# Kernel tuning notes

Measured on AMD Instinct MI355X. Metric: run time of the kernel, lower is better.

The kernel has to match this reference:

```python
import jax, jax.numpy as jnp
import numpy as np
import math

N_HEADS = 16

def _rope_tables(T, D, dtype):
    # inv_freq over even dims, emb = [freqs, freqs] -> [T, D]
    inv_freq = 1.0 / (10000.0 ** (jnp.arange(0, D, 2, dtype=jnp.float32) / D))
    freqs = jnp.arange(T, dtype=jnp.float32)[:, None] * inv_freq[None, :]  # [T, D/2]
    emb = jnp.concatenate([freqs, freqs], axis=-1)  # [T, D]
    return jnp.cos(emb).astype(dtype), jnp.sin(emb).astype(dtype)

def _rotate_half(x):
    d = x.shape[-1] // 2
    return jnp.concatenate([-x[..., d:], x[..., :d]], axis=-1)

def setup_inputs() -> dict:
    key = jax.random.key(0)
    ks = jax.random.split(key, 5)
    B, T, C = 2, 2048, 1024
    s = 1.0 / math.sqrt(C)
    return {
        "x": jax.random.normal(ks[0], (B, T, C), dtype=jnp.float32),
        "Wq": jax.random.normal(ks[1], (C, C), dtype=jnp.float32) * s,
        "Wk": jax.random.normal(ks[2], (C, C), dtype=jnp.float32) * s,
        "Wv": jax.random.normal(ks[3], (C, C), dtype=jnp.float32) * s,
        "Wo": jax.random.normal(ks[4], (C, C), dtype=jnp.float32) * s,
    }

def reference(x, Wq, Wk, Wv, Wo):
    B, T, C = x.shape
    H = N_HEADS
    D = C // H
    # QKV projections (torch Linear, bias=False: y = x @ W.T), split into heads
    def proj(W):
        return (x @ W.T).reshape(B, T, H, D).transpose(0, 2, 1, 3)  # [B,H,T,D]
    q, k, v = proj(Wq), proj(Wk), proj(Wv)
    # RoPE
    cos, sin = _rope_tables(T, D, x.dtype)  # [T,D] each, broadcast over B,H
    q = q * cos + _rotate_half(q) * sin
    k = k * cos + _rotate_half(k) * sin
    # scaled dot-product attention with causal mask
    scale = 1.0 / math.sqrt(D)
    attn = jnp.einsum('bhtd,bhsd->bhts', q, k) * scale  # [B,H,T,T]
    row = jnp.arange(T)[:, None]
    col = jnp.arange(T)[None, :]
    attn = jnp.where(col > row, -jnp.inf, attn)
    p = jax.nn.softmax(attn, axis=-1)
    out = jnp.einsum('bhts,bhsd->bhtd', p, v)  # [B,H,T,D]
    out = out.transpose(0, 2, 1, 3).reshape(B, T, C)
    return out @ Wo.T
```

## Files before the change

### kernel.cpp

```cpp
#include <hip/hip_runtime.h>
#include <hip/hip_bf16.h>


typedef __hip_bfloat16 bf16;
typedef __attribute__((ext_vector_type(8))) short bf16x8;
typedef __attribute__((ext_vector_type(4))) float f32x4;
typedef __attribute__((ext_vector_type(4))) short short4v;

#define MFMA16(a, b, c) __builtin_amdgcn_mfma_f32_16x16x32_bf16((a), (b), (c), 0, 0, 0)

constexpr int Bn = 2, Hn = 16, Tn = 2048, Dn = 64, Cn = 1024;
constexpr size_t NE = (size_t)Bn * Tn * Cn;
constexpr size_t WE = (size_t)Cn * Cn;
constexpr float QSCALE = 0.125f * 1.44269504088896f;
constexpr int PS = 68;

__device__ inline unsigned short bfbits(float x) {
    bf16 b = __float2bfloat16(x);
    return *(unsigned short*)&b;
}

__device__ inline bf16x8 pack8(f32x4 a, f32x4 b) {
    bf16x8 r;
#pragma unroll
    for (int i = 0; i < 4; ++i) r[i] = (short)bfbits(a[i]);
#pragma unroll
    for (int i = 0; i < 4; ++i) r[4 + i] = (short)bfbits(b[i]);
    return r;
}

__global__ __launch_bounds__(256) void convert_kernel(
    const float* __restrict__ x, const float* __restrict__ wq,
    const float* __restrict__ wk, const float* __restrict__ wv,
    const float* __restrict__ wo, bf16* __restrict__ dst)
{
    int blk = blockIdx.x;
    int lane = threadIdx.x & 63;
    int lx = lane & 15, quad = lane >> 4;
    const float* src;
    size_t doff;
    if (blk < 2048) {
        int frag = blk * 4 + (threadIdx.x >> 6);
        int mt = frag >> 5, kc = frag & 31;
        src = x + (size_t)(mt * 16 + lx) * Cn + kc * 32 + quad * 8;
        doff = (size_t)frag * 512 + lane * 8;
    } else {
        int w = (blk - 2048) >> 9, b = (blk - 2048) & 511;
        const float* s4[4] = {wq, wk, wv, wo};
        int frag = b * 4 + (threadIdx.x >> 6);
        int nb = frag >> 5, kc = frag & 31;
        src = s4[w] + (size_t)(nb * 16 + lx) * Cn + kc * 32 + quad * 8;
        doff = NE + (size_t)w * WE + (size_t)frag * 512 + lane * 8;
    }
    f32x4 a = *(const f32x4*)(src);
    f32x4 b2 = *(const f32x4*)(src + 4);
    *(bf16x8*)(dst + doff) = pack8(a, b2);
}

__global__ __launch_bounds__(256) void gemm_qkv_kernel(
    const bf16* __restrict__ Xf, const bf16* __restrict__ Wbase,
    bf16* __restrict__ Qo, bf16* __restrict__ Ko, bf16* __restrict__ Vo)
{
    const int bm = blockIdx.x, bn = blockIdx.y, wsel = blockIdx.z;
    const bf16* W = Wbase + (size_t)wsel * WE;
    const int tid  = threadIdx.x;
    const int wave = tid >> 6, lane = tid & 63;
    const int lx   = lane & 15, quad = lane >> 4;
    const int wm = wave >> 1, wn = wave & 1;

    const int mt0 = bm * 8 + wm * 4;
    const int nb0 = bn * 8 + wn * 4;
    const bf16* afrag = Xf + (size_t)mt0 * 32 * 512 + (size_t)lane * 8;
    const bf16* wfrag = W + (size_t)nb0 * 32 * 512 + (size_t)lane * 8;

    f32x4 acc[4][4] = {};
    bf16x8 acur[4], bcur[4], anxt[4], bnxt[4];
#pragma unroll
    for (int i = 0; i < 4; ++i) {
        acur[i] = *(const bf16x8*)(afrag + (size_t)i * 32 * 512);
        bcur[i] = *(const bf16x8*)(wfrag + (size_t)i * 32 * 512);
    }
    for (int kc = 0; kc < 32; ++kc) {
        if (kc < 31) {
#pragma unroll
            for (int i = 0; i < 4; ++i) {
                anxt[i] = *(const bf16x8*)(afrag + ((size_t)i * 32 + kc + 1) * 512);
                bnxt[i] = *(const bf16x8*)(wfrag + ((size_t)i * 32 + kc + 1) * 512);
            }
        }
#pragma unroll
        for (int mt = 0; mt < 4; ++mt)
#pragma unroll
            for (int nt = 0; nt < 4; ++nt)
                acc[mt][nt] = MFMA16(acur[mt], bcur[nt], acc[mt][nt]);
#pragma unroll
        for (int i = 0; i < 4; ++i) { acur[i] = anxt[i]; bcur[i] = bnxt[i]; }
    }

    const int h = bn * 2 + wn;
    if (wsel <= 1) {
#pragma unroll
        for (int mt = 0; mt < 4; ++mt)
#pragma unroll
            for (int r = 0; r < 4; ++r) {
                int mg = bm * 128 + wm * 64 + mt * 16 + quad * 4 + r;
                int t  = mg & (Tn - 1);
#pragma unroll
                for (int nt = 0; nt < 2; ++nt) {
                    int d = nt * 16 + lx;
                    float ang = (float)t * __expf(-(float)d * 0.2878231366f);
                    float c, s;
                    __sincosf(ang, &s, &c);
                    float a0 = acc[mt][nt][r], a1 = acc[mt][nt + 2][r];
                    acc[mt][nt][r]     = a0 * c - a1 * s;
                    acc[mt][nt + 2][r] = a1 * c + a0 * s;
                }
            }
    }

#pragma unroll
    for (int mt = 0; mt < 4; ++mt) {
        int mg0 = bm * 128 + wm * 64 + mt * 16 + quad * 4;
        int b = mg0 >> 11, tlo = mg0 & (Tn - 1);
        if (wsel == 0) {
#pragma unroll
            for (int nt = 0; nt < 4; ++nt)
#pragma unroll
                for (int r = 0; r < 4; ++r) {
                    int d = nt * 16 + lx;
                    Qo[((size_t)(b * Hn + h) * Tn + tlo + r) * Dn + d] =
                        __float2bfloat16(acc[mt][nt][r] * QSCALE);
                }
        } else if (wsel == 1) {
            bf16* Kf = Ko + (size_t)(b * Hn + h) * Tn * Dn;
            int c = tlo >> 6, ntk = (tlo >> 4) & 3;
#pragma unroll
            for (int nt = 0; nt < 4; ++nt) {
                size_t base = ((size_t)(c * 4 + ntk) * 2 + (nt >> 1)) * 512
                            + (size_t)((nt & 1) * 2 + (lx >> 3)) * 128
                            + (size_t)(tlo & 15) * 8 + (lx & 7);
#pragma unroll
                for (int r = 0; r < 4; ++r)
                    Kf[base + (size_t)r * 8] = __float2bfloat16(acc[mt][nt][r]);
            }
        } else {
            bf16* Vf = Vo + (size_t)(b * Hn + h) * Tn * Dn;
            int c = tlo >> 6, ksv = (tlo >> 5) & 1;
            int qv = (tlo >> 3) & 3, pos0 = tlo & 7;
#pragma unroll
            for (int nt = 0; nt < 4; ++nt) {
                short4v pk;
#pragma unroll
                for (int r = 0; r < 4; ++r) pk[r] = (short)bfbits(acc[mt][nt][r]);
                *(short4v*)&Vf[((size_t)(c * 8 + nt * 2 + ksv)) * 512
                               + (size_t)qv * 128 + (size_t)lx * 8 + pos0] = pk;
            }
        }
    }
}

__global__ __launch_bounds__(256) void gemm_out_kernel(
    const bf16* __restrict__ Af, const bf16* __restrict__ W, float* __restrict__ Out)
{
    const int bm = blockIdx.x, bn = blockIdx.y;
    const int tid  = threadIdx.x;
    const int wave = tid >> 6, lane = tid & 63;
    const int lx   = lane & 15, quad = lane >> 4;
    const int wm = wave >> 1, wn = wave & 1;

    const int mt0 = bm * 8 + wm * 4;
    const int nb0 = bn * 8 + wn * 4;
    const bf16* afrag = Af + (size_t)mt0 * 32 * 512 + (size_t)lane * 8;
    const bf16* wfrag = W + (size_t)nb0 * 32 * 512 + (size_t)lane * 8;

    f32x4 acc[4][4] = {};
    bf16x8 acur[4], bcur[4], anxt[4], bnxt[4];
#pragma unroll
    for (int i = 0; i < 4; ++i) {
        acur[i] = *(const bf16x8*)(afrag + (size_t)i * 32 * 512);
        bcur[i] = *(const bf16x8*)(wfrag + (size_t)i * 32 * 512);
    }
    for (int kc = 0; kc < 32; ++kc) {
        if (kc < 31) {
#pragma unroll
            for (int i = 0; i < 4; ++i) {
                anxt[i] = *(const bf16x8*)(afrag + ((size_t)i * 32 + kc + 1) * 512);
                bnxt[i] = *(const bf16x8*)(wfrag + ((size_t)i * 32 + kc + 1) * 512);
            }
        }
#pragma unroll
        for (int mt = 0; mt < 4; ++mt)
#pragma unroll
            for (int nt = 0; nt < 4; ++nt)
                acc[mt][nt] = MFMA16(acur[mt], bcur[nt], acc[mt][nt]);
#pragma unroll
        for (int i = 0; i < 4; ++i) { acur[i] = anxt[i]; bcur[i] = bnxt[i]; }
    }
#pragma unroll
    for (int mt = 0; mt < 4; ++mt)
#pragma unroll
        for (int nt = 0; nt < 4; ++nt)
#pragma unroll
            for (int r = 0; r < 4; ++r) {
                int mg = bm * 128 + wm * 64 + mt * 16 + quad * 4 + r;
                int ng = bn * 128 + wn * 64 + nt * 16 + lx;
                Out[(size_t)mg * Cn + ng] = acc[mt][nt][r];
            }
}

__global__ __launch_bounds__(256, 2) void attn_kernel(
    const bf16* __restrict__ Q, const bf16* __restrict__ K,
    const bf16* __restrict__ Vt, bf16* __restrict__ O)
{
    __shared__ unsigned short Pl[4][16 * PS];
    const int g  = blockIdx.x;
    const int bh = g & 31;
    const int p  = g >> 5;
    const int tHi = 31 - p, tLo = p;
    const int tid  = threadIdx.x;
    const int wave = tid >> 6, lane = tid & 63;
    const int lx   = lane & 15, quad = lane >> 4;

    const bf16* Qh = Q  + (size_t)bh * Tn * Dn;
    const bf16* Kh = K  + (size_t)bh * Tn * Dn;
    const bf16* Vh = Vt + (size_t)bh * Tn * Dn;
    unsigned short* pw = &Pl[wave][0];

    const int qrowH = tHi * 64 + wave * 16 + lx;
    bf16x8 aqH0 = *(const bf16x8*)(Qh + (size_t)qrowH * Dn + quad * 8);
    bf16x8 aqH1 = *(const bf16x8*)(Qh + (size_t)qrowH * Dn + 32 + quad * 8);
    const int qrowL = tLo * 64 + wave * 16 + lx;
    bf16x8 aqL0 = *(const bf16x8*)(Qh + (size_t)qrowL * Dn + quad * 8);
    bf16x8 aqL1 = *(const bf16x8*)(Qh + (size_t)qrowL * Dn + 32 + quad * 8);

    bf16x8 ones;
#pragma unroll
    for (int i = 0; i < 8; ++i) ones[i] = (short)0x3F80;

    f32x4 acc_oH[4] = {}, acc_oL[4] = {};
    f32x4 acc_lH = {},    acc_lL = {};
    const int row_local = wave * 16 + quad * 4;

    auto storeP = [&](const f32x4* accs, bool diag) {
        if (!diag) {
#pragma unroll
            for (int nt = 0; nt < 4; ++nt)
#pragma unroll
                for (int r = 0; r < 4; ++r)
                    pw[(quad * 4 + r) * PS + nt * 16 + lx] = bfbits(exp2f(accs[nt][r]));
        } else {
#pragma unroll
            for (int nt = 0; nt < 4; ++nt) {
                int keyl = nt * 16 + lx;
#pragma unroll
                for (int r = 0; r < 4; ++r) {
                    float pv = (keyl > row_local + r) ? 0.0f : exp2f(accs[nt][r]);
                    pw[(quad * 4 + r) * PS + nt * 16 + lx] = bfbits(pv);
                }
            }
        }
    };

    for (int c = 0; c <= tHi; ++c) {
        const bf16* kp = Kh + (size_t)c * 4096 + lane * 8;
        const bf16* vp = Vh + (size_t)c * 4096 + lane * 8;
        bf16x8 k[8], v[8];
#pragma unroll
        for (int i = 0; i < 8; ++i) {
            k[i] = *(const bf16x8*)(kp + (size_t)i * 512);
            v[i] = *(const bf16x8*)(vp + (size_t)i * 512);
        }
        const bool lo = (c <= tLo);
        f32x4 accsH[4] = {};
#pragma unroll
        for (int nt = 0; nt < 4; ++nt) {
            accsH[nt] = MFMA16(aqH0, k[nt * 2], accsH[nt]);
            accsH[nt] = MFMA16(aqH1, k[nt * 2 + 1], accsH[nt]);
        }
        f32x4 accsL[4] = {};
        if (lo) {
#pragma unroll
            for (int nt = 0; nt < 4; ++nt) {
                accsL[nt] = MFMA16(aqL0, k[nt * 2], accsL[nt]);
                accsL[nt] = MFMA16(aqL1, k[nt * 2 + 1], accsL[nt]);
            }
        }
        storeP(accsH, c == tHi);
        asm volatile("s_waitcnt lgkmcnt(0)" ::: "memory");
        {
            bf16x8 ap0 = *(const bf16x8*)&pw[lx * PS + quad * 8];
            bf16x8 ap1 = *(const bf16x8*)&pw[lx * PS + 32 + quad * 8];
            acc_lH = MFMA16(ap0, ones, acc_lH);
            acc_lH = MFMA16(ap1, ones, acc_lH);
#pragma unroll
            for (int dt = 0; dt < 4; ++dt) {
                acc_oH[dt] = MFMA16(ap0, v[dt * 2], acc_oH[dt]);
                acc_oH[dt] = MFMA16(ap1, v[dt * 2 + 1], acc_oH[dt]);
            }
        }
        if (lo) {
            storeP(accsL, c == tLo);
            asm volatile("s_waitcnt lgkmcnt(0)" ::: "memory");
            bf16x8 ap0 = *(const bf16x8*)&pw[lx * PS + quad * 8];
            bf16x8 ap1 = *(const bf16x8*)&pw[lx * PS + 32 + quad * 8];
            acc_lL = MFMA16(ap0, ones, acc_lL);
            acc_lL = MFMA16(ap1, ones, acc_lL);
#pragma unroll
            for (int dt = 0; dt < 4; ++dt) {
                acc_oL[dt] = MFMA16(ap0, v[dt * 2], acc_oL[dt]);
                acc_oL[dt] = MFMA16(ap1, v[dt * 2 + 1], acc_oL[dt]);
            }
        }
    }

    const int b = bh >> 4, h = bh & 15;
    auto writeO = [&](int t, const f32x4* acc_o, const f32x4& acc_l) {
        const int mtile = b * 128 + t * 4 + wave;
#pragma unroll
        for (int dt = 0; dt < 4; ++dt) {
            int ch = h * 64 + dt * 16 + lx;
            size_t base = ((size_t)mtile * 32 + (ch >> 5)) * 512
                        + (size_t)(((ch >> 3) & 3) * 16) * 8 + (ch & 7);
#pragma unroll
            for (int r = 0; r < 4; ++r) {
                float o = acc_o[dt][r] / acc_l[r];
                O[base + (size_t)(quad * 4 + r) * 8] = __float2bfloat16(o);
            }
        }
    };
    writeO(tHi, acc_oH, acc_lH);
    writeO(tLo, acc_oL, acc_lL);
}

extern "C" void kernel_launch(void* const* d_in, const int* in_sizes, int n_in,
                              void* d_out, int out_size, void* d_ws, size_t ws_size,
                              hipStream_t stream)
{
    const float* x  = (const float*)d_in[0];
    const float* Wq = (const float*)d_in[1];
    const float* Wk = (const float*)d_in[2];
    const float* Wv = (const float*)d_in[3];
    const float* Wo = (const float*)d_in[4];
    float* out = (float*)d_out;

    bf16* ws = (bf16*)d_ws;
    bf16* Xf = ws;
    bf16* Wb = ws + NE;
    bf16* Qb = ws + NE + 4 * WE;
    bf16* Kb = Qb + NE;
    bf16* Vb = Kb + NE;
    bf16* Ab = Xf;

    convert_kernel<<<4096, 256, 0, stream>>>(x, Wq, Wk, Wv, Wo, ws);
    gemm_qkv_kernel<<<dim3(32, 8, 3), 256, 0, stream>>>(Xf, Wb, Qb, Kb, Vb);
    attn_kernel<<<512, 256, 0, stream>>>(Qb, Kb, Vb, Ab);
    gemm_out_kernel<<<dim3(32, 8), 256, 0, stream>>>(Ab, Wb + 3 * WE, out);
}
```

Before: 178.0 us.

## Split attention KV loop across two wave groups with LDS reduction

```diff
diff --git a/kernel.cpp b/kernel.cpp
--- a/kernel.cpp
+++ b/kernel.cpp
@@ -14,6 +14,7 @@
 constexpr size_t WE = (size_t)Cn * Cn;
 constexpr float QSCALE = 0.125f * 1.44269504088896f;
 constexpr int PS = 68;
+constexpr int CS = 66;
 
 __device__ inline unsigned short bfbits(float x) {
     bf16 b = __float2bfloat16(x);
@@ -208,28 +209,31 @@
             }
 }
 
-__global__ __launch_bounds__(256, 2) void attn_kernel(
+__global__ __launch_bounds__(512, 4) void attn_kernel(
     const bf16* __restrict__ Q, const bf16* __restrict__ K,
     const bf16* __restrict__ Vt, bf16* __restrict__ O)
 {
-    __shared__ unsigned short Pl[4][16 * PS];
+    __shared__ unsigned short Pl[8][16 * PS];
+    __shared__ float Cb[4][16 * CS];
     const int g  = blockIdx.x;
     const int bh = g & 31;
     const int p  = g >> 5;
     const int tHi = 31 - p, tLo = p;
     const int tid  = threadIdx.x;
     const int wave = tid >> 6, lane = tid & 63;
+    const int w4   = wave & 3, half = wave >> 2;
     const int lx   = lane & 15, quad = lane >> 4;
 
     const bf16* Qh = Q  + (size_t)bh * Tn * Dn;
     const bf16* Kh = K  + (size_t)bh * Tn * Dn;
     const bf16* Vh = Vt + (size_t)bh * Tn * Dn;
     unsigned short* pw = &Pl[wave][0];
-
-    const int qrowH = tHi * 64 + wave * 16 + lx;
+    float* cb = &Cb[w4][0];
+
+    const int qrowH = tHi * 64 + w4 * 16 + lx;
     bf16x8 aqH0 = *(const bf16x8*)(Qh + (size_t)qrowH * Dn + quad * 8);
     bf16x8 aqH1 = *(const bf16x8*)(Qh + (size_t)qrowH * Dn + 32 + quad * 8);
-    const int qrowL = tLo * 64 + wave * 16 + lx;
+    const int qrowL = tLo * 64 + w4 * 16 + lx;
     bf16x8 aqL0 = *(const bf16x8*)(Qh + (size_t)qrowL * Dn + quad * 8);
     bf16x8 aqL1 = *(const bf16x8*)(Qh + (size_t)qrowL * Dn + 32 + quad * 8);
 
@@ -239,7 +243,7 @@
 
     f32x4 acc_oH[4] = {}, acc_oL[4] = {};
     f32x4 acc_lH = {},    acc_lL = {};
-    const int row_local = wave * 16 + quad * 4;
+    const int row_local = w4 * 16 + quad * 4;
 
     auto storeP = [&](const f32x4* accs, bool diag) {
         if (!diag) {
@@ -261,7 +265,7 @@
         }
     };
 
-    for (int c = 0; c <= tHi; ++c) {
+    for (int c = half; c <= tHi; c += 2) {
         const bf16* kp = Kh + (size_t)c * 4096 + lane * 8;
         const bf16* vp = Vh + (size_t)c * 4096 + lane * 8;
         bf16x8 k[8], v[8];
@@ -286,7 +290,6 @@
             }
         }
         storeP(accsH, c == tHi);
-        asm volatile("s_waitcnt lgkmcnt(0)" ::: "memory");
         {
             bf16x8 ap0 = *(const bf16x8*)&pw[lx * PS + quad * 8];
             bf16x8 ap1 = *(const bf16x8*)&pw[lx * PS + 32 + quad * 8];
@@ -300,7 +303,6 @@
         }
         if (lo) {
             storeP(accsL, c == tLo);
-            asm volatile("s_waitcnt lgkmcnt(0)" ::: "memory");
             bf16x8 ap0 = *(const bf16x8*)&pw[lx * PS + quad * 8];
             bf16x8 ap1 = *(const bf16x8*)&pw[lx * PS + 32 + quad * 8];
             acc_lL = MFMA16(ap0, ones, acc_lL);
@@ -315,7 +317,7 @@
 
     const int b = bh >> 4, h = bh & 15;
     auto writeO = [&](int t, const f32x4* acc_o, const f32x4& acc_l) {
-        const int mtile = b * 128 + t * 4 + wave;
+        const int mtile = b * 128 + t * 4 + w4;
 #pragma unroll
         for (int dt = 0; dt < 4; ++dt) {
             int ch = h * 64 + dt * 16 + lx;
@@ -328,8 +330,35 @@
             }
         }
     };
-    writeO(tHi, acc_oH, acc_lH);
-    writeO(tLo, acc_oL, acc_lL);
+    auto putC = [&](const f32x4* acc_o, const f32x4& acc_l) {
+#pragma unroll
+        for (int dt = 0; dt < 4; ++dt)
+#pragma unroll
+            for (int r = 0; r < 4; ++r)
+                cb[(quad * 4 + r) * CS + dt * 16 + lx] = acc_o[dt][r];
+        if (lx == 0)
+#pragma unroll
+            for (int r = 0; r < 4; ++r)
+                cb[(quad * 4 + r) * CS + 64] = acc_l[r];
+    };
+    auto addC = [&](f32x4* acc_o, f32x4& acc_l) {
+#pragma unroll
+        for (int dt = 0; dt < 4; ++dt)
+#pragma unroll
+            for (int r = 0; r < 4; ++r)
+                acc_o[dt][r] += cb[(quad * 4 + r) * CS + dt * 16 + lx];
+#pragma unroll
+        for (int r = 0; r < 4; ++r)
+            acc_l[r] += cb[(quad * 4 + r) * CS + 64];
+    };
+
+    if (half == 1) putC(acc_oH, acc_lH);
+    __syncthreads();
+    if (half == 0) { addC(acc_oH, acc_lH); writeO(tHi, acc_oH, acc_lH); }
+    __syncthreads();
+    if (half == 1) putC(acc_oL, acc_lL);
+    __syncthreads();
+    if (half == 0) { addC(acc_oL, acc_lL); writeO(tLo, acc_oL, acc_lL); }
 }
 
 extern "C" void kernel_launch(void* const* d_in, const int* in_sizes, int n_in,
@@ -353,6 +382,6 @@
 
     convert_kernel<<<4096, 256, 0, stream>>>(x, Wq, Wk, Wv, Wo, ws);
     gemm_qkv_kernel<<<dim3(32, 8, 3), 256, 0, stream>>>(Xf, Wb, Qb, Kb, Vb);
-    attn_kernel<<<512, 256, 0, stream>>>(Qb, Kb, Vb, Ab);
+    attn_kernel<<<512, 512, 0, stream>>>(Qb, Kb, Vb, Ab);
     gemm_out_kernel<<<dim3(32, 8), 256, 0, stream>>>(Ab, Wb + 3 * WE, out);
 }
```

New measurement: 241.5 us. +35.7%, slower.

## Split attention KV loop across two blocks and combine partials in a separate kernel

Applied to the files above, without the earlier changes.

```diff
diff --git a/kernel.cpp b/kernel.cpp
--- a/kernel.cpp
+++ b/kernel.cpp
@@ -208,14 +208,16 @@
             }
 }
 
-__global__ __launch_bounds__(256, 2) void attn_kernel(
+__global__ __launch_bounds__(256, 4) void attn_kernel(
     const bf16* __restrict__ Q, const bf16* __restrict__ K,
-    const bf16* __restrict__ Vt, bf16* __restrict__ O)
+    const bf16* __restrict__ Vt, float* __restrict__ Opart,
+    float* __restrict__ lpart)
 {
     __shared__ unsigned short Pl[4][16 * PS];
     const int g  = blockIdx.x;
     const int bh = g & 31;
-    const int p  = g >> 5;
+    const int p  = (g >> 5) & 15;
+    const int s  = g >> 9;
     const int tHi = 31 - p, tLo = p;
     const int tid  = threadIdx.x;
     const int wave = tid >> 6, lane = tid & 63;
@@ -261,7 +263,7 @@
         }
     };
 
-    for (int c = 0; c <= tHi; ++c) {
+    for (int c = s; c <= tHi; c += 2) {
         const bf16* kp = Kh + (size_t)c * 4096 + lane * 8;
         const bf16* vp = Vh + (size_t)c * 4096 + lane * 8;
         bf16x8 k[8], v[8];
@@ -313,23 +315,49 @@
         }
     }
 
+    const int pairIdx = g & 511;
+    float* Op = Opart + ((size_t)pairIdx * 2 + s) * 8192;
+    float* lp = lpart + ((size_t)pairIdx * 2 + s) * 128;
+    auto storePart = [&](int roff, const f32x4* acc_o, const f32x4& acc_l) {
+#pragma unroll
+        for (int dt = 0; dt < 4; ++dt)
+#pragma unroll
+            for (int r = 0; r < 4; ++r)
+                Op[(size_t)(roff + wave * 16 + quad * 4 + r) * 64 + dt * 16 + lx]
+                    = acc_o[dt][r];
+        if (lx == 0)
+#pragma unroll
+            for (int r = 0; r < 4; ++r)
+                lp[roff + wave * 16 + quad * 4 + r] = acc_l[r];
+    };
+    storePart(0, acc_oH, acc_lH);
+    storePart(64, acc_oL, acc_lL);
+}
+
+__global__ __launch_bounds__(256) void attn_combine_kernel(
+    const float* __restrict__ Opart, const float* __restrict__ lpart,
+    bf16* __restrict__ O)
+{
+    const int pair = blockIdx.x;
+    const int bh = pair & 31, p = pair >> 5;
+    const int tHi = 31 - p, tLo = p;
     const int b = bh >> 4, h = bh & 15;
-    auto writeO = [&](int t, const f32x4* acc_o, const f32x4& acc_l) {
-        const int mtile = b * 128 + t * 4 + wave;
-#pragma unroll
-        for (int dt = 0; dt < 4; ++dt) {
-            int ch = h * 64 + dt * 16 + lx;
-            size_t base = ((size_t)mtile * 32 + (ch >> 5)) * 512
-                        + (size_t)(((ch >> 3) & 3) * 16) * 8 + (ch & 7);
-#pragma unroll
-            for (int r = 0; r < 4; ++r) {
-                float o = acc_o[dt][r] / acc_l[r];
-                O[base + (size_t)(quad * 4 + r) * 8] = __float2bfloat16(o);
-            }
-        }
-    };
-    writeO(tHi, acc_oH, acc_lH);
-    writeO(tLo, acc_oL, acc_lL);
+    const float* O0 = Opart + (size_t)pair * 2 * 8192;
+    const float* O1 = O0 + 8192;
+    const float* l0 = lpart + (size_t)pair * 2 * 128;
+    const float* l1 = l0 + 128;
+    for (int idx = threadIdx.x; idx < 8192; idx += 256) {
+        int row = idx >> 6, ch = idx & 63;
+        float l = l0[row] + l1[row];
+        float o = (O0[idx] + O1[idx]) / l;
+        int t  = (row < 64) ? tHi : tLo;
+        int rl = row & 63;
+        int mtile = b * 128 + t * 4 + (rl >> 4);
+        int chg = h * 64 + ch;
+        size_t base = ((size_t)mtile * 32 + (chg >> 5)) * 512
+                    + (size_t)(((chg >> 3) & 3) * 16) * 8 + (chg & 7);
+        O[base + (size_t)(rl & 15) * 8] = __float2bfloat16(o);
+    }
 }
 
 extern "C" void kernel_launch(void* const* d_in, const int* in_sizes, int n_in,
@@ -350,9 +378,12 @@
     bf16* Kb = Qb + NE;
     bf16* Vb = Kb + NE;
     bf16* Ab = Xf;
+    float* Opart = (float*)(ws + 4 * NE + 4 * WE);
+    float* lpart = Opart + (size_t)512 * 2 * 8192;
 
     convert_kernel<<<4096, 256, 0, stream>>>(x, Wq, Wk, Wv, Wo, ws);
     gemm_qkv_kernel<<<dim3(32, 8, 3), 256, 0, stream>>>(Xf, Wb, Qb, Kb, Vb);
-    attn_kernel<<<512, 256, 0, stream>>>(Qb, Kb, Vb, Ab);
+    attn_kernel<<<1024, 256, 0, stream>>>(Qb, Kb, Vb, Opart, lpart);
+    attn_combine_kernel<<<512, 256, 0, stream>>>(Opart, lpart, Ab);
     gemm_out_kernel<<<dim3(32, 8), 256, 0, stream>>>(Ab, Wb + 3 * WE, out);
 }
```

New measurement: 241.4 us. +35.7%, slower.
